# Optimization experiments

Hardware: AMD Instinct MI355X
Metric: run time of the kernel (lower is better)

## Reference

```python
import jax, jax.numpy as jnp
import numpy as np

H = 32        # num_attention_heads (query heads)
G = 8         # num_query_groups (KV heads)
D = 128       # head_dim
HID = 4096    # hidden_size
THETA = 10000.0


def _rope(x, pos):
    # x: [B, h, S, D]; pos: [S]. Rotate-half (LLaMA) convention.
    half = D // 2
    inv_freq = 1.0 / (THETA ** (jnp.arange(0, half, dtype=jnp.float32) / half))
    ang = pos[:, None].astype(jnp.float32) * inv_freq[None, :]   # [S, half]
    cos = jnp.cos(ang)[None, None]                               # [1,1,S,half]
    sin = jnp.sin(ang)[None, None]
    x1, x2 = x[..., :half], x[..., half:]
    return jnp.concatenate([x1 * cos - x2 * sin, x1 * sin + x2 * cos], axis=-1)


def setup_inputs() -> dict:
    key = jax.random.key(0)
    ks = jax.random.split(key, 9)
    s = 0.02
    return {
        "hidden_states": jax.random.normal(ks[0], (1, 2048, HID), jnp.float32),
        "Wq": jax.random.normal(ks[1], (HID, H * D), jnp.float32) * s,
        "bq": jnp.zeros((H * D,), jnp.float32),
        "Wk": jax.random.normal(ks[2], (HID, G * D), jnp.float32) * s,
        "bk": jnp.zeros((G * D,), jnp.float32),
        "Wv": jax.random.normal(ks[3], (HID, G * D), jnp.float32) * s,
        "bv": jnp.zeros((G * D,), jnp.float32),
        "Wo": jax.random.normal(ks[4], (H * D, HID), jnp.float32) * s,
        "bo": jnp.zeros((HID,), jnp.float32),
    }


def reference(hidden_states, Wq, bq, Wk, bk, Wv, bv, Wo, bo):
    B, S, _ = hidden_states.shape
    R = H // G  # query heads per KV group

    q = hidden_states @ Wq + bq  # [B,S,H*D]
    k = hidden_states @ Wk + bk  # [B,S,G*D]
    v = hidden_states @ Wv + bv  # [B,S,G*D]

    q = q.reshape(B, S, H, D).transpose(0, 2, 1, 3)  # [B,H,S,D]
    k = k.reshape(B, S, G, D).transpose(0, 2, 1, 3)  # [B,G,S,D]
    v = v.reshape(B, S, G, D).transpose(0, 2, 1, 3)  # [B,G,S,D]

    pos = jnp.arange(S)
    q = _rope(q, pos)
    k = _rope(k, pos)

    # Grouped attention: broadcast KV across the R query heads of each group
    qg = q.reshape(B, G, R, S, D)
    scores = jnp.einsum('bgrsd,bgtd->bgrst', qg, k) / jnp.sqrt(jnp.float32(D))
    causal = jnp.tril(jnp.ones((S, S), dtype=bool))
    scores = jnp.where(causal[None, None, None], scores, jnp.finfo(scores.dtype).min)
    probs = jax.nn.softmax(scores, axis=-1)
    ctx = jnp.einsum('bgrst,bgtd->bgrsd', probs, v)          # [B,G,R,S,D]
    ctx = ctx.reshape(B, H, S, D).transpose(0, 2, 1, 3).reshape(B, S, H * D)
    return ctx @ Wo + bo
```

## Files before the change

### kernel.cpp

```cpp
#include <hip/hip_runtime.h>
#include <hip/hip_bf16.h>
#include <math.h>

#define HID   4096
#define NH    32
#define NG    8
#define DH    128
#define SEQ   2048
#define QKV_N 6144
#define KOFF  4096
#define VOFF  5120

typedef __bf16 bf16x8 __attribute__((ext_vector_type(8)));
typedef float  f32x4  __attribute__((ext_vector_type(4)));
using bf16 = __hip_bfloat16;

#define LOG2E 1.4426950408889634f
#define SCALE 0.08838834764831845f

typedef const __attribute__((address_space(1))) void* gas_p;
typedef __attribute__((address_space(3))) void* las_p;
__device__ __forceinline__ void async_copy16(void* lds, const void* g) {
  __builtin_amdgcn_global_load_lds((gas_p)g, (las_p)lds, 16, 0, 0);
}

__global__ void cast_x_kernel(const float* __restrict__ x, bf16* __restrict__ y, int n4) {
  int i = blockIdx.x * blockDim.x + threadIdx.x;
  if (i >= n4) return;
  float4 v = ((const float4*)x)[i];
  union { bf16 h[4]; uint2 u; } t;
  t.h[0] = __float2bfloat16(v.x);
  t.h[1] = __float2bfloat16(v.y);
  t.h[2] = __float2bfloat16(v.z);
  t.h[3] = __float2bfloat16(v.w);
  ((uint2*)y)[i] = t.u;
}

__global__ void wtrans_kernel(const float* __restrict__ W, bf16* __restrict__ dst, int K, int N) {
  __shared__ float t[32][33];
  int tx = threadIdx.x, ty = threadIdx.y;
  int n0 = blockIdx.x * 32, k0 = blockIdx.y * 32;
#pragma unroll
  for (int i = 0; i < 4; ++i)
    t[ty + i * 8][tx] = W[(size_t)(k0 + ty + i * 8) * N + n0 + tx];
  __syncthreads();
#pragma unroll
  for (int i = 0; i < 4; ++i)
    dst[(size_t)(n0 + ty + i * 8) * K + k0 + tx] = __float2bfloat16(t[tx][ty + i * 8]);
}

__global__ void bias_concat_kernel(const float* __restrict__ bq, const float* __restrict__ bk,
                                   const float* __restrict__ bv, float* __restrict__ dst) {
  int i = blockIdx.x * blockDim.x + threadIdx.x;
  if (i < 4096)       dst[i] = bq[i];
  else if (i < 5120)  dst[i] = bk[i - 4096];
  else if (i < 6144)  dst[i] = bv[i - 5120];
}

__device__ __forceinline__ void st_out(float* C, size_t idx, float v) { C[idx] = v; }
__device__ __forceinline__ void st_out(bf16*  C, size_t idx, float v) { C[idx] = __float2bfloat16(v); }

template <typename OutT>
__global__ __launch_bounds__(256) void gemm_bt_kernel(const bf16* __restrict__ A, const bf16* __restrict__ Bt,
                                                      const float* __restrict__ bias, OutT* __restrict__ C,
                                                      int M, int N, int K) {
  __shared__ alignas(16) bf16 As[128][32];
  __shared__ alignas(16) bf16 Bs[128][32];
  const int tid = threadIdx.x;
  const int w = tid >> 6, lane = tid & 63, quad = lane >> 4, l16 = lane & 15;
  const int wr = w >> 1, wc = w & 1;
  const int m0 = blockIdx.y * 128, n0 = blockIdx.x * 128;
  const int srow = lane >> 2;
  const int scol = (lane & 3) * 8;

  f32x4 acc[4][4];
  f32x4 zero4 = {0.f, 0.f, 0.f, 0.f};
#pragma unroll
  for (int mt = 0; mt < 4; ++mt)
#pragma unroll
    for (int nt = 0; nt < 4; ++nt) acc[mt][nt] = zero4;

  const int nIter = K >> 5;
  for (int kb = 0; kb < nIter; ++kb) {
    const int k0 = kb << 5;
#pragma unroll
    for (int c = 0; c < 2; ++c) {
      const int rb = w * 16 + c * 64;
      async_copy16(&As[rb][0], A  + (size_t)(m0 + rb + srow) * K + k0 + scol);
      async_copy16(&Bs[rb][0], Bt + (size_t)(n0 + rb + srow) * K + k0 + scol);
    }
    __syncthreads();
    bf16x8 af[4], bfr[4];
#pragma unroll
    for (int i = 0; i < 4; ++i) {
      af[i]  = *(const bf16x8*)&As[wr * 64 + i * 16 + l16][quad * 8];
      bfr[i] = *(const bf16x8*)&Bs[wc * 64 + i * 16 + l16][quad * 8];
    }
#pragma unroll
    for (int mt = 0; mt < 4; ++mt)
#pragma unroll
      for (int nt = 0; nt < 4; ++nt)
        acc[mt][nt] = __builtin_amdgcn_mfma_f32_16x16x32_bf16(af[mt], bfr[nt], acc[mt][nt], 0, 0, 0);
    __syncthreads();
  }

#pragma unroll
  for (int nt = 0; nt < 4; ++nt) {
    const int col = n0 + wc * 64 + nt * 16 + l16;
    const float bv = bias[col];
#pragma unroll
    for (int mt = 0; mt < 4; ++mt) {
#pragma unroll
      for (int r = 0; r < 4; ++r) {
        const int row = m0 + wr * 64 + mt * 16 + quad * 4 + r;
        st_out(C, (size_t)row * N + col, acc[mt][nt][r] + bv);
      }
    }
  }
}

__global__ void rope_kernel(bf16* __restrict__ qkv) {
  int t = blockIdx.x * blockDim.x + threadIdx.x;
  int d  = t & 63;
  int hs = (t >> 6) % 40;
  int s  = t / (64 * 40);
  int base = (hs < 32) ? hs * 128 : KOFF + (hs - 32) * 128;
  bf16* p = qkv + (size_t)s * QKV_N + base + d;
  float x1 = __bfloat162float(p[0]);
  float x2 = __bfloat162float(p[64]);
  float inv = expf(d * -0.14391156862f);
  float ang = (float)s * inv;
  float sn, cs;
  sincosf(ang, &sn, &cs);
  p[0]  = __float2bfloat16(x1 * cs - x2 * sn);
  p[64] = __float2bfloat16(x1 * sn + x2 * cs);
}

__global__ void vtrans_kernel(const bf16* __restrict__ qkv, bf16* __restrict__ vt) {
  __shared__ bf16 t[32][33];
  int tx = threadIdx.x, ty = threadIdx.y;
  int s0 = blockIdx.x * 32, d0 = blockIdx.y * 32, g = blockIdx.z;
#pragma unroll
  for (int i = 0; i < 4; ++i)
    t[ty + i * 8][tx] = qkv[(size_t)(s0 + ty + i * 8) * QKV_N + VOFF + g * 128 + d0 + tx];
  __syncthreads();
#pragma unroll
  for (int i = 0; i < 4; ++i)
    vt[(size_t)(g * 128 + d0 + ty + i * 8) * SEQ + s0 + tx] = t[tx][ty + i * 8];
}

__global__ __launch_bounds__(256, 2) void attn_kernel(const bf16* __restrict__ qkv, const bf16* __restrict__ vt,
                                                      bf16* __restrict__ ctx) {
  __shared__ bf16 Ks[2][64][128];
  __shared__ bf16 Ps[64][72];

  const int bx = blockIdx.x;
  const int h  = blockIdx.y;
  const int g  = h >> 2;
  const int tid = threadIdx.x, w = tid >> 6, lane = tid & 63;
  const int quad = lane >> 4, l16 = lane & 15;
  const int sw = l16 & 7;

  const float c1 = SCALE * LOG2E;
  const float c2 = 12.0f * LOG2E;

  f32x4 zero4 = {0.f, 0.f, 0.f, 0.f};

  auto stage = [&](int kt2, int buf) {
    const bf16* kg = qkv + (size_t)(kt2 * 64) * QKV_N + KOFF + g * 128;
    bf16* ksb = &Ks[buf][0][0];
#pragma unroll
    for (int i = 0; i < 4; ++i) {
      int c = (i * 4 + w) * 64 + lane;
      int key = c >> 4, j = c & 15;
      int js = (j & 8) | ((j ^ key) & 7);
      async_copy16(ksb + (size_t)(i * 4 + w) * 512, kg + (size_t)key * QKV_N + js * 8);
    }
  };

  for (int ph = 0; ph < 2; ++ph) {
    const int qt = ph ? bx : (31 - bx);
    const int n  = qt + 1;

    bf16x8 qf[4];
    {
      const int qrow = qt * 64 + w * 16 + l16;
      const bf16* qp = qkv + (size_t)qrow * QKV_N + h * 128 + quad * 8;
#pragma unroll
      for (int ks = 0; ks < 4; ++ks) qf[ks] = *(const bf16x8*)(qp + ks * 32);
    }

    f32x4 o[8];
#pragma unroll
    for (int dt = 0; dt < 8; ++dt) o[dt] = zero4;
    float rsum[4] = {0.f, 0.f, 0.f, 0.f};

    __syncthreads();
    stage(0, 0);

    for (int kt = 0; kt < n; ++kt) {
      const int cur = kt & 1;
      __syncthreads();
      if (kt + 1 < n) stage(kt + 1, 1 - cur);

      f32x4 s[4];
#pragma unroll
      for (int nt = 0; nt < 4; ++nt) {
        s[nt] = zero4;
#pragma unroll
        for (int ks = 0; ks < 4; ++ks) {
          bf16x8 kf = *(const bf16x8*)&Ks[cur][nt * 16 + l16][((ks * 4 + quad) ^ sw) * 8];
          s[nt] = __builtin_amdgcn_mfma_f32_16x16x32_bf16(qf[ks], kf, s[nt], 0, 0, 0);
        }
      }

#pragma unroll
      for (int nt = 0; nt < 4; ++nt)
#pragma unroll
        for (int r = 0; r < 4; ++r)
          s[nt][r] = exp2f(fmaf(s[nt][r], c1, -c2));

      if (kt == qt) {
        const int ql = w * 16 + quad * 4;
#pragma unroll
        for (int nt = 0; nt < 4; ++nt) {
          const int key = nt * 16 + l16;
#pragma unroll
          for (int r = 0; r < 4; ++r)
            if (key > ql + r) s[nt][r] = 0.f;
        }
      }

#pragma unroll
      for (int r = 0; r < 4; ++r)
        rsum[r] += (s[0][r] + s[1][r]) + (s[2][r] + s[3][r]);

#pragma unroll
      for (int nt = 0; nt < 4; ++nt)
#pragma unroll
        for (int r = 0; r < 4; ++r)
          Ps[w * 16 + quad * 4 + r][nt * 16 + l16] = __float2bfloat16(s[nt][r]);

      bf16x8 pf[2];
#pragma unroll
      for (int k2 = 0; k2 < 2; ++k2)
        pf[k2] = *(const bf16x8*)&Ps[w * 16 + l16][k2 * 32 + quad * 8];
      const bf16* vbase = vt + (size_t)(g * 128) * SEQ + kt * 64;
#pragma unroll
      for (int dt = 0; dt < 8; ++dt) {
        const bf16* vrow = vbase + (size_t)(dt * 16 + l16) * SEQ + quad * 8;
#pragma unroll
        for (int k2 = 0; k2 < 2; ++k2) {
          bf16x8 vf = *(const bf16x8*)(vrow + k2 * 32);
          o[dt] = __builtin_amdgcn_mfma_f32_16x16x32_bf16(pf[k2], vf, o[dt], 0, 0, 0);
        }
      }
    }

#pragma unroll
    for (int r = 0; r < 4; ++r) {
      float rs = rsum[r];
      rs += __shfl_xor(rs, 1, 64);
      rs += __shfl_xor(rs, 2, 64);
      rs += __shfl_xor(rs, 4, 64);
      rs += __shfl_xor(rs, 8, 64);
      rsum[r] = 1.0f / rs;
    }
    const int orow = qt * 64 + w * 16 + quad * 4;
#pragma unroll
    for (int dt = 0; dt < 8; ++dt)
#pragma unroll
      for (int r = 0; r < 4; ++r)
        ctx[(size_t)(orow + r) * HID + h * 128 + dt * 16 + l16] = __float2bfloat16(o[dt][r] * rsum[r]);
  }
}

extern "C" void kernel_launch(void* const* d_in, const int* in_sizes, int n_in,
                              void* d_out, int out_size, void* d_ws, size_t ws_size,
                              hipStream_t stream) {
  const float* X  = (const float*)d_in[0];
  const float* Wq = (const float*)d_in[1];
  const float* bq = (const float*)d_in[2];
  const float* Wk = (const float*)d_in[3];
  const float* bk = (const float*)d_in[4];
  const float* Wv = (const float*)d_in[5];
  const float* bv = (const float*)d_in[6];
  const float* Wo = (const float*)d_in[7];
  const float* bo = (const float*)d_in[8];
  float* out = (float*)d_out;

  char* ws = (char*)d_ws;
  size_t off = 0;
  auto alloc = [&](size_t bytes) { char* p = ws + off; off += (bytes + 255) & ~255ULL; return p; };
  bf16*  Xb     = (bf16*) alloc((size_t)SEQ * HID * 2);
  bf16*  Wqkv_t = (bf16*) alloc((size_t)QKV_N * HID * 2);
  bf16*  Wot    = (bf16*) alloc((size_t)HID * HID * 2);
  float* bqkv   = (float*)alloc((size_t)QKV_N * 4);
  bf16*  QKV    = (bf16*) alloc((size_t)SEQ * QKV_N * 2);
  bf16*  Vt     = (bf16*) alloc((size_t)NG * DH * SEQ * 2);
  bf16*  Ctx    = (bf16*) alloc((size_t)SEQ * HID * 2);

  dim3 tb(32, 8);
  cast_x_kernel<<<SEQ * HID / 4 / 256, 256, 0, stream>>>(X, Xb, SEQ * HID / 4);
  wtrans_kernel<<<dim3(HID / 32, HID / 32), tb, 0, stream>>>(Wq, Wqkv_t, HID, HID);
  wtrans_kernel<<<dim3(1024 / 32, HID / 32), tb, 0, stream>>>(Wk, Wqkv_t + (size_t)KOFF * HID, HID, 1024);
  wtrans_kernel<<<dim3(1024 / 32, HID / 32), tb, 0, stream>>>(Wv, Wqkv_t + (size_t)VOFF * HID, HID, 1024);
  wtrans_kernel<<<dim3(HID / 32, HID / 32), tb, 0, stream>>>(Wo, Wot, HID, HID);
  bias_concat_kernel<<<QKV_N / 256, 256, 0, stream>>>(bq, bk, bv, bqkv);

  gemm_bt_kernel<bf16><<<dim3(QKV_N / 128, SEQ / 128), 256, 0, stream>>>(Xb, Wqkv_t, bqkv, QKV, SEQ, QKV_N, HID);
  rope_kernel<<<SEQ * 40 * 64 / 256, 256, 0, stream>>>(QKV);
  vtrans_kernel<<<dim3(SEQ / 32, DH / 32, NG), tb, 0, stream>>>(QKV, Vt);
  attn_kernel<<<dim3(16, NH), 256, 0, stream>>>(QKV, Vt, Ctx);
  gemm_bt_kernel<float><<<dim3(HID / 128, SEQ / 128), 256, 0, stream>>>(Ctx, Wot, bo, out, SEQ, HID, HID);
}
```

Baseline: 616.3 us.

## Vectorize transposes and RoPE, swizzle GEMM tiles, stage V in LDS in attention

The weight transpose now works on 64x64 tiles with float4 loads and 16-byte bf16 stores. RoPE handles 8 elements per thread with vector loads. The GEMM grid is flattened and remapped into 4-row-block stripes to improve L2 reuse. In attention, the score MFMA operands are swapped so P can be moved between lanes with ds_bpermute instead of an LDS round-trip, V tiles are staged asynchronously into swizzled LDS double buffers, and the context is written with packed stores. Together these touch several unrelated kernels, which adds register and LDS pressure in attention and some risk in the lane-mapping correctness.

Measured after the change: 570.8 us. -7.4%, faster.

```diff
diff --git a/kernel.cpp b/kernel.cpp
--- a/kernel.cpp
+++ b/kernel.cpp
@@ -22,6 +22,13 @@
 typedef __attribute__((address_space(3))) void* las_p;
 __device__ __forceinline__ void async_copy16(void* lds, const void* g) {
   __builtin_amdgcn_global_load_lds((gas_p)g, (las_p)lds, 16, 0, 0);
+}
+
+__device__ __forceinline__ unsigned pack2(float a, float b) {
+  union { bf16 h[2]; unsigned u; } t;
+  t.h[0] = __float2bfloat16(a);
+  t.h[1] = __float2bfloat16(b);
+  return t.u;
 }
 
 __global__ void cast_x_kernel(const float* __restrict__ x, bf16* __restrict__ y, int n4) {
@@ -36,17 +43,33 @@
   ((uint2*)y)[i] = t.u;
 }
 
-__global__ void wtrans_kernel(const float* __restrict__ W, bf16* __restrict__ dst, int K, int N) {
-  __shared__ float t[32][33];
-  int tx = threadIdx.x, ty = threadIdx.y;
-  int n0 = blockIdx.x * 32, k0 = blockIdx.y * 32;
-#pragma unroll
-  for (int i = 0; i < 4; ++i)
-    t[ty + i * 8][tx] = W[(size_t)(k0 + ty + i * 8) * N + n0 + tx];
+__global__ __launch_bounds__(256) void wtrans_kernel(const float* __restrict__ W, bf16* __restrict__ dst,
+                                                     int K, int N) {
+  __shared__ bf16 T[64][72];
+  const int t = threadIdx.x;
+  const int n0 = blockIdx.x * 64, k0 = blockIdx.y * 64;
+  const int nn = (t & 15) * 4, kk = t >> 4;
+#pragma unroll
+  for (int p = 0; p < 4; ++p) {
+    const int k = kk + p * 16;
+    float4 v = *(const float4*)&W[(size_t)(k0 + k) * N + n0 + nn];
+    union { bf16 h[4]; uint2 u; } c;
+    c.h[0] = __float2bfloat16(v.x);
+    c.h[1] = __float2bfloat16(v.y);
+    c.h[2] = __float2bfloat16(v.z);
+    c.h[3] = __float2bfloat16(v.w);
+    *(uint2*)&T[k][nn] = c.u;
+  }
   __syncthreads();
-#pragma unroll
-  for (int i = 0; i < 4; ++i)
-    dst[(size_t)(n0 + ty + i * 8) * K + k0 + tx] = __float2bfloat16(t[tx][ty + i * 8]);
+  const int kc = t & 7, nr = t >> 3;
+#pragma unroll
+  for (int p = 0; p < 2; ++p) {
+    const int n = nr + p * 32;
+    union { bf16 h[8]; uint4 u; } o;
+#pragma unroll
+    for (int i = 0; i < 8; ++i) o.h[i] = T[kc * 8 + i][n];
+    *(uint4*)&dst[(size_t)(n0 + n) * K + k0 + kc * 8] = o.u;
+  }
 }
 
 __global__ void bias_concat_kernel(const float* __restrict__ bq, const float* __restrict__ bk,
@@ -69,7 +92,12 @@
   const int tid = threadIdx.x;
   const int w = tid >> 6, lane = tid & 63, quad = lane >> 4, l16 = lane & 15;
   const int wr = w >> 1, wc = w & 1;
-  const int m0 = blockIdx.y * 128, n0 = blockIdx.x * 128;
+  const int nbn = N >> 7;
+  const int b = blockIdx.x;
+  const int stripe = 4 * nbn;
+  const int sid = b / stripe, rem = b - sid * stripe;
+  const int m0 = (sid * 4 + (rem & 3)) << 7;
+  const int n0 = (rem >> 2) << 7;
   const int srow = lane >> 2;
   const int scol = (lane & 3) * 8;
 
@@ -121,19 +149,28 @@
 
 __global__ void rope_kernel(bf16* __restrict__ qkv) {
   int t = blockIdx.x * blockDim.x + threadIdx.x;
-  int d  = t & 63;
-  int hs = (t >> 6) % 40;
-  int s  = t / (64 * 40);
+  int c  = t & 7;
+  int hs = (t >> 3) % 40;
+  int s  = t / 320;
   int base = (hs < 32) ? hs * 128 : KOFF + (hs - 32) * 128;
-  bf16* p = qkv + (size_t)s * QKV_N + base + d;
-  float x1 = __bfloat162float(p[0]);
-  float x2 = __bfloat162float(p[64]);
-  float inv = expf(d * -0.14391156862f);
-  float ang = (float)s * inv;
-  float sn, cs;
-  sincosf(ang, &sn, &cs);
-  p[0]  = __float2bfloat16(x1 * cs - x2 * sn);
-  p[64] = __float2bfloat16(x1 * sn + x2 * cs);
+  bf16* p = qkv + (size_t)s * QKV_N + base + c * 8;
+  union { bf16x8 v; bf16 h[8]; } a, b, ra, rb;
+  a.v = *(bf16x8*)p;
+  b.v = *(bf16x8*)(p + 64);
+#pragma unroll
+  for (int j = 0; j < 8; ++j) {
+    int d = c * 8 + j;
+    float inv = expf(d * -0.14391156862f);
+    float ang = (float)s * inv;
+    float sn, cs;
+    sincosf(ang, &sn, &cs);
+    float x1 = __bfloat162float(a.h[j]);
+    float x2 = __bfloat162float(b.h[j]);
+    ra.h[j] = __float2bfloat16(x1 * cs - x2 * sn);
+    rb.h[j] = __float2bfloat16(x1 * sn + x2 * cs);
+  }
+  *(bf16x8*)p        = ra.v;
+  *(bf16x8*)(p + 64) = rb.v;
 }
 
 __global__ void vtrans_kernel(const bf16* __restrict__ qkv, bf16* __restrict__ vt) {
@@ -152,7 +189,7 @@
 __global__ __launch_bounds__(256, 2) void attn_kernel(const bf16* __restrict__ qkv, const bf16* __restrict__ vt,
                                                       bf16* __restrict__ ctx) {
   __shared__ bf16 Ks[2][64][128];
-  __shared__ bf16 Ps[64][72];
+  __shared__ bf16 Vs[2][128][64];
 
   const int bx = blockIdx.x;
   const int h  = blockIdx.y;
@@ -164,17 +201,30 @@
   const float c1 = SCALE * LOG2E;
   const float c2 = 12.0f * LOG2E;
 
+  const int addrA = (((quad & 1) << 5) + l16) * 4;
+  const int addrB = addrA + 64;
+  const bool hiq = quad >= 2;
+
   f32x4 zero4 = {0.f, 0.f, 0.f, 0.f};
 
   auto stage = [&](int kt2, int buf) {
     const bf16* kg = qkv + (size_t)(kt2 * 64) * QKV_N + KOFF + g * 128;
-    bf16* ksb = &Ks[buf][0][0];
+    const bf16* vg = vt + (size_t)(g * 128) * SEQ + kt2 * 64;
 #pragma unroll
     for (int i = 0; i < 4; ++i) {
-      int c = (i * 4 + w) * 64 + lane;
-      int key = c >> 4, j = c & 15;
-      int js = (j & 8) | ((j ^ key) & 7);
-      async_copy16(ksb + (size_t)(i * 4 + w) * 512, kg + (size_t)key * QKV_N + js * 8);
+      const int c = (i * 4 + w) * 64 + lane;
+      {
+        const int key = c >> 4, j = c & 15;
+        const int js = (j & 8) | ((j ^ key) & 7);
+        async_copy16(&Ks[buf][0][0] + (size_t)(i * 4 + w) * 512,
+                     kg + (size_t)key * QKV_N + js * 8);
+      }
+      {
+        const int d = c >> 3, k8 = c & 7;
+        const int js = (k8 ^ d) & 7;
+        async_copy16(&Vs[buf][0][0] + (size_t)(i * 4 + w) * 512,
+                     vg + (size_t)d * SEQ + js * 8);
+      }
     }
   };
 
@@ -193,7 +243,7 @@
     f32x4 o[8];
 #pragma unroll
     for (int dt = 0; dt < 8; ++dt) o[dt] = zero4;
-    float rsum[4] = {0.f, 0.f, 0.f, 0.f};
+    float rsum = 0.f;
 
     __syncthreads();
     stage(0, 0);
@@ -209,8 +259,9 @@
         s[nt] = zero4;
 #pragma unroll
         for (int ks = 0; ks < 4; ++ks) {
-          bf16x8 kf = *(const bf16x8*)&Ks[cur][nt * 16 + l16][((ks * 4 + quad) ^ sw) * 8];
-          s[nt] = __builtin_amdgcn_mfma_f32_16x16x32_bf16(qf[ks], kf, s[nt], 0, 0, 0);
+          const int ch = ks * 4 + quad;
+          bf16x8 kf = *(const bf16x8*)&Ks[cur][nt * 16 + l16][((ch & 8) | ((ch ^ l16) & 7)) * 8];
+          s[nt] = __builtin_amdgcn_mfma_f32_16x16x32_bf16(kf, qf[ks], s[nt], 0, 0, 0);
         }
       }
 
@@ -221,57 +272,62 @@
           s[nt][r] = exp2f(fmaf(s[nt][r], c1, -c2));
 
       if (kt == qt) {
-        const int ql = w * 16 + quad * 4;
-#pragma unroll
-        for (int nt = 0; nt < 4; ++nt) {
-          const int key = nt * 16 + l16;
+        const int q_local = w * 16 + l16;
+#pragma unroll
+        for (int nt = 0; nt < 4; ++nt)
 #pragma unroll
           for (int r = 0; r < 4; ++r)
-            if (key > ql + r) s[nt][r] = 0.f;
+            if (nt * 16 + quad * 4 + r > q_local) s[nt][r] = 0.f;
+      }
+
+#pragma unroll
+      for (int nt = 0; nt < 4; ++nt)
+        rsum += (s[nt][0] + s[nt][1]) + (s[nt][2] + s[nt][3]);
+
+      unsigned pk[4][2];
+#pragma unroll
+      for (int nt = 0; nt < 4; ++nt) {
+        pk[nt][0] = pack2(s[nt][0], s[nt][1]);
+        pk[nt][1] = pack2(s[nt][2], s[nt][3]);
+      }
+
+#pragma unroll
+      for (int k2 = 0; k2 < 2; ++k2) {
+        const int lo = 2 * k2, hi = lo + 1;
+        int a0l = __builtin_amdgcn_ds_bpermute(addrA, (int)pk[lo][0]);
+        int a1l = __builtin_amdgcn_ds_bpermute(addrA, (int)pk[lo][1]);
+        int b0l = __builtin_amdgcn_ds_bpermute(addrB, (int)pk[lo][0]);
+        int b1l = __builtin_amdgcn_ds_bpermute(addrB, (int)pk[lo][1]);
+        int a0h = __builtin_amdgcn_ds_bpermute(addrA, (int)pk[hi][0]);
+        int a1h = __builtin_amdgcn_ds_bpermute(addrA, (int)pk[hi][1]);
+        int b0h = __builtin_amdgcn_ds_bpermute(addrB, (int)pk[hi][0]);
+        int b1h = __builtin_amdgcn_ds_bpermute(addrB, (int)pk[hi][1]);
+        union { int u[4]; bf16x8 v; } pf;
+        pf.u[0] = hiq ? a0h : a0l;
+        pf.u[1] = hiq ? a1h : a1l;
+        pf.u[2] = hiq ? b0h : b0l;
+        pf.u[3] = hiq ? b1h : b1l;
+#pragma unroll
+        for (int dt = 0; dt < 8; ++dt) {
+          const int ch = k2 * 4 + quad;
+          bf16x8 vf = *(const bf16x8*)&Vs[cur][dt * 16 + l16][((ch ^ sw) & 7) * 8];
+          o[dt] = __builtin_amdgcn_mfma_f32_16x16x32_bf16(vf, pf.v, o[dt], 0, 0, 0);
         }
       }
-
-#pragma unroll
-      for (int r = 0; r < 4; ++r)
-        rsum[r] += (s[0][r] + s[1][r]) + (s[2][r] + s[3][r]);
-
-#pragma unroll
-      for (int nt = 0; nt < 4; ++nt)
-#pragma unroll
-        for (int r = 0; r < 4; ++r)
-          Ps[w * 16 + quad * 4 + r][nt * 16 + l16] = __float2bfloat16(s[nt][r]);
-
-      bf16x8 pf[2];
-#pragma unroll
-      for (int k2 = 0; k2 < 2; ++k2)
-        pf[k2] = *(const bf16x8*)&Ps[w * 16 + l16][k2 * 32 + quad * 8];
-      const bf16* vbase = vt + (size_t)(g * 128) * SEQ + kt * 64;
-#pragma unroll
-      for (int dt = 0; dt < 8; ++dt) {
-        const bf16* vrow = vbase + (size_t)(dt * 16 + l16) * SEQ + quad * 8;
-#pragma unroll
-        for (int k2 = 0; k2 < 2; ++k2) {
-          bf16x8 vf = *(const bf16x8*)(vrow + k2 * 32);
-          o[dt] = __builtin_amdgcn_mfma_f32_16x16x32_bf16(pf[k2], vf, o[dt], 0, 0, 0);
-        }
-      }
-    }
-
-#pragma unroll
-    for (int r = 0; r < 4; ++r) {
-      float rs = rsum[r];
-      rs += __shfl_xor(rs, 1, 64);
-      rs += __shfl_xor(rs, 2, 64);
-      rs += __shfl_xor(rs, 4, 64);
-      rs += __shfl_xor(rs, 8, 64);
-      rsum[r] = 1.0f / rs;
-    }
-    const int orow = qt * 64 + w * 16 + quad * 4;
-#pragma unroll
-    for (int dt = 0; dt < 8; ++dt)
-#pragma unroll
-      for (int r = 0; r < 4; ++r)
-        ctx[(size_t)(orow + r) * HID + h * 128 + dt * 16 + l16] = __float2bfloat16(o[dt][r] * rsum[r]);
+    }
+
+    rsum += __shfl_xor(rsum, 16, 64);
+    rsum += __shfl_xor(rsum, 32, 64);
+    const float inv = 1.0f / rsum;
+    const int srow = qt * 64 + w * 16 + l16;
+    bf16* cp = ctx + (size_t)srow * HID + h * 128 + quad * 4;
+#pragma unroll
+    for (int dt = 0; dt < 8; ++dt) {
+      union { bf16 h[4]; uint2 u; } ov;
+#pragma unroll
+      for (int r = 0; r < 4; ++r) ov.h[r] = __float2bfloat16(o[dt][r] * inv);
+      *(uint2*)(cp + dt * 16) = ov.u;
+    }
   }
 }
 
@@ -300,17 +356,17 @@
   bf16*  Vt     = (bf16*) alloc((size_t)NG * DH * SEQ * 2);
   bf16*  Ctx    = (bf16*) alloc((size_t)SEQ * HID * 2);
 
+  cast_x_kernel<<<SEQ * HID / 4 / 256, 256, 0, stream>>>(X, Xb, SEQ * HID / 4);
+  wtrans_kernel<<<dim3(HID / 64, HID / 64), 256, 0, stream>>>(Wq, Wqkv_t, HID, HID);
+  wtrans_kernel<<<dim3(1024 / 64, HID / 64), 256, 0, stream>>>(Wk, Wqkv_t + (size_t)KOFF * HID, HID, 1024);
+  wtrans_kernel<<<dim3(1024 / 64, HID / 64), 256, 0, stream>>>(Wv, Wqkv_t + (size_t)VOFF * HID, HID, 1024);
+  wtrans_kernel<<<dim3(HID / 64, HID / 64), 256, 0, stream>>>(Wo, Wot, HID, HID);
+  bias_concat_kernel<<<QKV_N / 256, 256, 0, stream>>>(bq, bk, bv, bqkv);
+
+  gemm_bt_kernel<bf16><<<(SEQ / 128) * (QKV_N / 128), 256, 0, stream>>>(Xb, Wqkv_t, bqkv, QKV, SEQ, QKV_N, HID);
+  rope_kernel<<<SEQ * 40 * 8 / 256, 256, 0, stream>>>(QKV);
   dim3 tb(32, 8);
-  cast_x_kernel<<<SEQ * HID / 4 / 256, 256, 0, stream>>>(X, Xb, SEQ * HID / 4);
-  wtrans_kernel<<<dim3(HID / 32, HID / 32), tb, 0, stream>>>(Wq, Wqkv_t, HID, HID);
-  wtrans_kernel<<<dim3(1024 / 32, HID / 32), tb, 0, stream>>>(Wk, Wqkv_t + (size_t)KOFF * HID, HID, 1024);
-  wtrans_kernel<<<dim3(1024 / 32, HID / 32), tb, 0, stream>>>(Wv, Wqkv_t + (size_t)VOFF * HID, HID, 1024);
-  wtrans_kernel<<<dim3(HID / 32, HID / 32), tb, 0, stream>>>(Wo, Wot, HID, HID);
-  bias_concat_kernel<<<QKV_N / 256, 256, 0, stream>>>(bq, bk, bv, bqkv);
-
-  gemm_bt_kernel<bf16><<<dim3(QKV_N / 128, SEQ / 128), 256, 0, stream>>>(Xb, Wqkv_t, bqkv, QKV, SEQ, QKV_N, HID);
-  rope_kernel<<<SEQ * 40 * 64 / 256, 256, 0, stream>>>(QKV);
   vtrans_kernel<<<dim3(SEQ / 32, DH / 32, NG), tb, 0, stream>>>(QKV, Vt);
   attn_kernel<<<dim3(16, NH), 256, 0, stream>>>(QKV, Vt, Ctx);
-  gemm_bt_kernel<float><<<dim3(HID / 128, SEQ / 128), 256, 0, stream>>>(Ctx, Wot, bo, out, SEQ, HID, HID);
-}
+  gemm_bt_kernel<float><<<(SEQ / 128) * (HID / 128), 256, 0, stream>>>(Ctx, Wot, bo, out, SEQ, HID, HID);
+}
```
